# Optimization experiments

Hardware: AMD Instinct MI355X
Metric: run time of the kernel (lower is better)

Reference implementation:

```python
import jax, jax.numpy as jnp
import numpy as np

B, S, D = 32, 256, 768
H = 12
HD = D // H           # 64
MLP = 4 * D           # 3072
EPS = 1e-5


def layernorm(x, g, b):
    mu = jnp.mean(x, axis=-1, keepdims=True)
    var = jnp.mean((x - mu) ** 2, axis=-1, keepdims=True)
    return (x - mu) * jax.lax.rsqrt(var + EPS) * g + b


def setup_inputs() -> dict:
    key = jax.random.key(0)
    ks = jax.random.split(key, 16)
    s_head = 1.0 / np.sqrt(HD)
    s_d = 1.0 / np.sqrt(D)
    s_mlp = 1.0 / np.sqrt(MLP)
    return {
        "x": jax.random.normal(ks[0], (B, S, D), dtype=jnp.float32),
        "g1": jnp.ones((D,), jnp.float32),
        "beta1": jnp.zeros((D,), jnp.float32),
        # per-head linear weights, torch Linear layout [out, in] stacked over heads
        "Wq": jax.random.uniform(ks[1], (H, HD, HD), jnp.float32, -s_head, s_head),
        "bq": jax.random.uniform(ks[2], (H, HD), jnp.float32, -s_head, s_head),
        "Wk": jax.random.uniform(ks[3], (H, HD, HD), jnp.float32, -s_head, s_head),
        "bk": jax.random.uniform(ks[4], (H, HD), jnp.float32, -s_head, s_head),
        "Wv": jax.random.uniform(ks[5], (H, HD, HD), jnp.float32, -s_head, s_head),
        "bv": jax.random.uniform(ks[6], (H, HD), jnp.float32, -s_head, s_head),
        "g2": jnp.ones((D,), jnp.float32),
        "beta2": jnp.zeros((D,), jnp.float32),
        "W1": jax.random.uniform(ks[7], (MLP, D), jnp.float32, -s_d, s_d),
        "bm1": jax.random.uniform(ks[8], (MLP,), jnp.float32, -s_d, s_d),
        "W2": jax.random.uniform(ks[9], (D, MLP), jnp.float32, -s_mlp, s_mlp),
        "bm2": jax.random.uniform(ks[10], (D,), jnp.float32, -s_mlp, s_mlp),
    }


def reference(x, g1, beta1, Wq, bq, Wk, bk, Wv, bv, g2, beta2, W1, bm1, W2, bm2):
    # --- MHA on norm1(x), fused over batch and heads ---
    h = layernorm(x, g1, beta1)                      # [B,S,D]
    hh = h.reshape(B, S, H, HD)                      # head split matches slicing in Mymha
    # q_e = sum_d hh_d * W[e,d]  (torch Linear: y = x @ W.T + b)
    q = jnp.einsum('bshd,hed->bshe', hh, Wq) + bq
    k = jnp.einsum('bshd,hed->bshe', hh, Wk) + bk
    v = jnp.einsum('bshd,hed->bshe', hh, Wv) + bv
    scores = jnp.einsum('bshe,bthe->bhst', q, k) / np.sqrt(HD)
    attn = jax.nn.softmax(scores, axis=-1)           # [B,H,S,S]
    ctx = jnp.einsum('bhst,bthe->bshe', attn, v).reshape(B, S, D)
    out = ctx + x
    # --- MLP on norm2(out) ---
    h2 = layernorm(out, g2, beta2)
    m = jax.nn.gelu(h2 @ W1.T + bm1, approximate=False)  # torch nn.GELU is exact erf
    out = m @ W2.T + bm2 + out
    return out
```

## Files before the change

### kernel.cpp

```cpp
#include <hip/hip_runtime.h>
#include <hip/hip_bf16.h>
#include <math.h>


static constexpr int Bn = 32, Sn = 256, Dn = 768, Hn = 12, HDn = 64, MLPn = 3072;
static constexpr int NT = Bn * Sn;

typedef unsigned short ushort_t;
typedef unsigned int u32;
typedef __attribute__((ext_vector_type(8))) short short8;
typedef __attribute__((ext_vector_type(4))) float f32x4;

__device__ __forceinline__ float bf2f(ushort_t u) { return __uint_as_float(((u32)u) << 16); }
__device__ __forceinline__ ushort_t f2bf(float f) {
  u32 u = __float_as_uint(f);
  u += 0x7fffu + ((u >> 16) & 1u);
  return (ushort_t)(u >> 16);
}

__device__ __forceinline__ void async_cp16(const ushort_t* g, ushort_t* l) {
  __builtin_amdgcn_global_load_lds(
      (const __attribute__((address_space(1))) u32*)g,
      (__attribute__((address_space(3))) u32*)l, 16, 0, 0);
}

__global__ __launch_bounds__(256) void k_prep(
    const float* __restrict__ Wq, const float* __restrict__ Wk,
    const float* __restrict__ Wv, const float* __restrict__ bq,
    const float* __restrict__ bk, const float* __restrict__ bv,
    const float* __restrict__ W1, const float* __restrict__ W2,
    const float* __restrict__ x, const float* __restrict__ g1,
    const float* __restrict__ be1,
    ushort_t* __restrict__ Wc, float* __restrict__ bc,
    ushort_t* __restrict__ W1b, ushort_t* __restrict__ W2b,
    ushort_t* __restrict__ hb)
{
  __shared__ float red[8];
  const int bx = blockIdx.x;
  const int tid = threadIdx.x;
  if (bx < 576) {
    int i = bx * 256 + tid;
    int h = i / 12288, rem = i - h * 12288;
    int mat = rem / 4096, w = rem - mat * 4096;
    const float* src = (mat == 0) ? Wq : ((mat == 1) ? Wk : Wv);
    Wc[i] = f2bf(src[h * 4096 + w]);
    if (i < Hn * 192) {
      int h2 = i / 192, r2 = i - h2 * 192;
      int m2 = r2 / 64, e2 = r2 - m2 * 64;
      const float* bs = (m2 == 0) ? bq : ((m2 == 1) ? bk : bv);
      bc[i] = bs[h2 * 64 + e2];
    }
  } else if (bx < 5184) {
    int j = bx - 576;
    const float* src = (j < 2304) ? W1 : W2;
    ushort_t* dst = (j < 2304) ? W1b : W2b;
    int i = (j % 2304) * 256 + tid;
    float4 v = ((const float4*)src)[i];
    ushort4 o;
    o.x = f2bf(v.x); o.y = f2bf(v.y); o.z = f2bf(v.z); o.w = f2bf(v.w);
    ((ushort4*)dst)[i] = o;
  } else {
    const int t = bx - 5184;
    float xv[3];
#pragma unroll
    for (int i = 0; i < 3; i++) xv[i] = x[(size_t)t * Dn + tid + i * 256];
    float s = xv[0] + xv[1] + xv[2];
#pragma unroll
    for (int off = 32; off > 0; off >>= 1) s += __shfl_down(s, off, 64);
    if ((tid & 63) == 0) red[tid >> 6] = s;
    __syncthreads();
    float mean = (red[0] + red[1] + red[2] + red[3]) * (1.0f / 768.0f);
    float d0 = xv[0] - mean, d1 = xv[1] - mean, d2 = xv[2] - mean;
    float s2 = d0 * d0 + d1 * d1 + d2 * d2;
#pragma unroll
    for (int off = 32; off > 0; off >>= 1) s2 += __shfl_down(s2, off, 64);
    if ((tid & 63) == 0) red[4 + (tid >> 6)] = s2;
    __syncthreads();
    float rstd = rsqrtf((red[4] + red[5] + red[6] + red[7]) * (1.0f / 768.0f) + 1e-5f);
#pragma unroll
    for (int i = 0; i < 3; i++) {
      int d = tid + i * 256;
      hb[(size_t)t * Dn + d] = f2bf((xv[i] - mean) * rstd * g1[d] + be1[d]);
    }
  }
}

__global__ __launch_bounds__(256) void k_qkv(
    const ushort_t* __restrict__ hb,
    const ushort_t* __restrict__ Wc,
    const float* __restrict__ bc,
    ushort_t* __restrict__ qo, ushort_t* __restrict__ ko, ushort_t* __restrict__ vt)
{
  __shared__ __align__(16) ushort_t As[128 * 72];
  __shared__ __align__(16) ushort_t Ws[192 * 72];
  const int blk = blockIdx.x;
  const int half = blk & 1;
  const int bh = blk >> 1;
  const int b_ = bh / Hn, h_ = bh - b_ * Hn;
  const int tid = threadIdx.x;
  const int t0 = b_ * Sn + half * 128;

  {
    int row = tid >> 1, seg = (tid & 1) * 32;
    const uint4* g = (const uint4*)(hb + (size_t)(t0 + row) * Dn + h_ * 64 + seg);
    uint4* s = (uint4*)(As + row * 72 + seg);
    s[0] = g[0]; s[1] = g[1]; s[2] = g[2]; s[3] = g[3];
  }
  {
    int rr = tid >> 2, seg = (tid & 3) * 16;
    const ushort_t* gw = Wc + h_ * 12288;
#pragma unroll
    for (int p = 0; p < 3; p++) {
      int R = p * 64 + rr;
      const uint4* g = (const uint4*)(gw + R * 64 + seg);
      uint4* s = (uint4*)(Ws + R * 72 + seg);
      s[0] = g[0]; s[1] = g[1];
    }
  }
  __syncthreads();

  const int wave = tid >> 6, lane = tid & 63;
  const int wm = (wave >> 1) * 64, wn = (wave & 1) * 96;
  const int lrow = lane & 15, quad = lane >> 4;

  f32x4 acc[4][6];
#pragma unroll
  for (int mi = 0; mi < 4; mi++)
#pragma unroll
    for (int ni = 0; ni < 6; ni++) acc[mi][ni] = (f32x4){0.f, 0.f, 0.f, 0.f};

#pragma unroll
  for (int kk = 0; kk < 2; kk++) {
    short8 af[4], wf[6];
#pragma unroll
    for (int mi = 0; mi < 4; mi++)
      af[mi] = *(const short8*)(As + (wm + mi * 16 + lrow) * 72 + kk * 32 + quad * 8);
#pragma unroll
    for (int ni = 0; ni < 6; ni++)
      wf[ni] = *(const short8*)(Ws + (wn + ni * 16 + lrow) * 72 + kk * 32 + quad * 8);
#pragma unroll
    for (int mi = 0; mi < 4; mi++)
#pragma unroll
      for (int ni = 0; ni < 6; ni++)
        acc[mi][ni] = __builtin_amdgcn_mfma_f32_16x16x32_bf16(af[mi], wf[ni], acc[mi][ni], 0, 0, 0);
  }

#pragma unroll
  for (int ni = 0; ni < 6; ni++) {
    int c = wn + ni * 16 + lrow;
    int mat = c >> 6, e = c & 63;
    float bb = bc[h_ * 192 + c];
    if (mat < 2) {
      ushort_t* dst = (mat == 0) ? qo : ko;
      size_t base = (((size_t)bh) * Sn + half * 128 + wm) * HDn + e;
#pragma unroll
      for (int mi = 0; mi < 4; mi++) {
#pragma unroll
        for (int r = 0; r < 4; r++) {
          int lr = mi * 16 + quad * 4 + r;
          dst[base + (size_t)lr * HDn] = f2bf(acc[mi][ni][r] + bb);
        }
      }
    } else {
      size_t rowb = ((size_t)bh * 64 + e) * Sn + half * 128 + wm + quad * 4;
#pragma unroll
      for (int mi = 0; mi < 4; mi++) {
        ushort4 pk;
        pk.x = f2bf(acc[mi][ni][0] + bb);
        pk.y = f2bf(acc[mi][ni][1] + bb);
        pk.z = f2bf(acc[mi][ni][2] + bb);
        pk.w = f2bf(acc[mi][ni][3] + bb);
        *(ushort4*)(vt + rowb + mi * 16) = pk;
      }
    }
  }
}

__global__ __launch_bounds__(256) void k_attn(
    const ushort_t* __restrict__ q,
    const ushort_t* __restrict__ kg_,
    const ushort_t* __restrict__ vt,
    const float* __restrict__ x,
    float* __restrict__ out1)
{
  __shared__ __align__(16) ushort_t Ks[64 * 72];
  __shared__ __align__(16) ushort_t Vts[64 * 264];
  __shared__ __align__(16) ushort_t Pw[4][16 * 72];
  const int blk = blockIdx.x;
  const int qtr = blk & 3, bh = blk >> 2;
  const int b_ = bh / Hn, h_ = bh - b_ * Hn;
  const int tid = threadIdx.x, wave = tid >> 6, lane = tid & 63;
  const int lr16 = lane & 15, quad = lane >> 4;
  const int s0 = qtr * 64 + wave * 16;

  {
    int r = tid >> 2, cseg = (tid & 3) * 64;
    const uint4* g = (const uint4*)(vt + ((size_t)bh * 64 + r) * Sn + cseg);
    uint4* s = (uint4*)(Vts + r * 264 + cseg);
#pragma unroll
    for (int i = 0; i < 8; i++) s[i] = g[i];
  }

  short8 qf[2];
  {
    const ushort_t* qg = q + ((size_t)bh * Sn + s0 + lr16) * HDn + quad * 8;
    qf[0] = *(const short8*)(qg);
    qf[1] = *(const short8*)(qg + 32);
  }

  f32x4 of[4];
#pragma unroll
  for (int et = 0; et < 4; et++) of[et] = (f32x4){0.f, 0.f, 0.f, 0.f};
  float mrow[4] = {-3.0e38f, -3.0e38f, -3.0e38f, -3.0e38f};
  float lsum[4] = {0.f, 0.f, 0.f, 0.f};

  const ushort_t* kgb = kg_ + (size_t)bh * Sn * HDn;

  for (int c = 0; c < 4; c++) {
    if (c) __syncthreads();
    {
      int row = tid >> 2, seg = (tid & 3) * 16;
      const uint4* g = (const uint4*)(kgb + (size_t)(c * 64 + row) * HDn + seg);
      uint4* s = (uint4*)(Ks + row * 72 + seg);
      s[0] = g[0]; s[1] = g[1];
    }
    __syncthreads();

    f32x4 sc[4];
#pragma unroll
    for (int ni = 0; ni < 4; ni++) sc[ni] = (f32x4){0.f, 0.f, 0.f, 0.f};
#pragma unroll
    for (int kk = 0; kk < 2; kk++) {
#pragma unroll
      for (int ni = 0; ni < 4; ni++) {
        short8 kf = *(const short8*)(Ks + (ni * 16 + lr16) * 72 + kk * 32 + quad * 8);
        sc[ni] = __builtin_amdgcn_mfma_f32_16x16x32_bf16(qf[kk], kf, sc[ni], 0, 0, 0);
      }
    }

    float alpha[4];
#pragma unroll
    for (int r = 0; r < 4; r++) {
      float m_ = fmaxf(fmaxf(sc[0][r], sc[1][r]), fmaxf(sc[2][r], sc[3][r]));
#pragma unroll
      for (int msk = 8; msk >= 1; msk >>= 1) m_ = fmaxf(m_, __shfl_xor(m_, msk, 64));
      float mn = fmaxf(mrow[r], m_);
      alpha[r] = __expf((mrow[r] - mn) * 0.125f);
      mrow[r] = mn;
    }
#pragma unroll
    for (int ni = 0; ni < 4; ni++) {
#pragma unroll
      for (int r = 0; r < 4; r++) {
        float p = __expf((sc[ni][r] - mrow[r]) * 0.125f);
        sc[ni][r] = p;
        Pw[wave][(quad * 4 + r) * 72 + ni * 16 + lr16] = f2bf(p);
      }
    }
#pragma unroll
    for (int r = 0; r < 4; r++) {
      float s_ = (sc[0][r] + sc[1][r]) + (sc[2][r] + sc[3][r]);
#pragma unroll
      for (int msk = 8; msk >= 1; msk >>= 1) s_ += __shfl_xor(s_, msk, 64);
      lsum[r] = lsum[r] * alpha[r] + s_;
    }
#pragma unroll
    for (int et = 0; et < 4; et++)
#pragma unroll
      for (int r = 0; r < 4; r++) of[et][r] *= alpha[r];

    short8 pf0 = *(const short8*)(&Pw[wave][lr16 * 72 + quad * 8]);
    short8 pf1 = *(const short8*)(&Pw[wave][lr16 * 72 + 32 + quad * 8]);
#pragma unroll
    for (int et = 0; et < 4; et++) {
      short8 vf0 = *(const short8*)(Vts + (et * 16 + lr16) * 264 + c * 64 + quad * 8);
      short8 vf1 = *(const short8*)(Vts + (et * 16 + lr16) * 264 + c * 64 + 32 + quad * 8);
      of[et] = __builtin_amdgcn_mfma_f32_16x16x32_bf16(pf0, vf0, of[et], 0, 0, 0);
      of[et] = __builtin_amdgcn_mfma_f32_16x16x32_bf16(pf1, vf1, of[et], 0, 0, 0);
    }
  }

  const size_t obase = ((size_t)b_ * Sn + s0) * Dn + h_ * 64;
#pragma unroll
  for (int r = 0; r < 4; r++) {
    float rl = 1.0f / lsum[r];
    int row = quad * 4 + r;
#pragma unroll
    for (int et = 0; et < 4; et++) {
      size_t idx = obase + (size_t)row * Dn + et * 16 + lr16;
      out1[idx] = of[et][r] * rl + x[idx];
    }
  }
}

__global__ __launch_bounds__(256) void k_ln2(
    const float* __restrict__ in, const float* __restrict__ g2,
    const float* __restrict__ be2, ushort_t* __restrict__ h2)
{
  const int t = blockIdx.x, tid = threadIdx.x;
  __shared__ float red[8];
  float xv[3];
#pragma unroll
  for (int i = 0; i < 3; i++) xv[i] = in[(size_t)t * Dn + tid + i * 256];
  float s = xv[0] + xv[1] + xv[2];
#pragma unroll
  for (int off = 32; off > 0; off >>= 1) s += __shfl_down(s, off, 64);
  if ((tid & 63) == 0) red[tid >> 6] = s;
  __syncthreads();
  float mean = (red[0] + red[1] + red[2] + red[3]) * (1.0f / 768.0f);
  float d0 = xv[0] - mean, d1 = xv[1] - mean, d2 = xv[2] - mean;
  float s2 = d0 * d0 + d1 * d1 + d2 * d2;
#pragma unroll
  for (int off = 32; off > 0; off >>= 1) s2 += __shfl_down(s2, off, 64);
  if ((tid & 63) == 0) red[4 + (tid >> 6)] = s2;
  __syncthreads();
  float rstd = rsqrtf((red[4] + red[5] + red[6] + red[7]) * (1.0f / 768.0f) + 1e-5f);
#pragma unroll
  for (int i = 0; i < 3; i++) {
    int d = tid + i * 256;
    h2[(size_t)t * Dn + d] = f2bf((xv[i] - mean) * rstd * g2[d] + be2[d]);
  }
}

__global__ __launch_bounds__(512) void k_gemm1(
    const ushort_t* __restrict__ A,
    const ushort_t* __restrict__ Bw,
    const float* __restrict__ bias,
    ushort_t* __restrict__ CoutB)
{
  constexpr int KDIM = Dn, N = MLPn;
  __shared__ __align__(16) ushort_t smem[24576];
  ushort_t* Asb[2] = { smem, smem + 12288 };
  ushort_t* Bsb[2] = { smem + 8192, smem + 20480 };
  ushort_t* Cs = smem;
  const int b = blockIdx.x;
  const int xcd = b & 7, slot = b >> 3;
  const int cc = slot % 24, rloc = slot / 24;
  const int m0 = (xcd * 4 + rloc) * 256, n0 = cc * 128;
  const int tid = threadIdx.x;
  const int wave = tid >> 6, lane = tid & 63;
  const int wm = (wave >> 1) << 6, wn = (wave & 1) << 6;
  const int lrow = lane & 15, quad = lane >> 4;
  const int lrow4 = lane >> 2, lcol8 = (lane & 3) * 8;

  f32x4 acc[4][4];
#pragma unroll
  for (int mi = 0; mi < 4; mi++)
#pragma unroll
    for (int ni = 0; ni < 4; ni++) acc[mi][ni] = (f32x4){0.f, 0.f, 0.f, 0.f};

  for (int k0 = 0; k0 < KDIM; k0 += 64) {
#pragma unroll
    for (int t = 0; t < 2; t++) {
      async_cp16(A + (size_t)(m0 + wave * 16 + lrow4) * KDIM + k0 + t * 32 + lcol8,
                 Asb[t] + (wave * 16) * 32);
      async_cp16(A + (size_t)(m0 + 128 + wave * 16 + lrow4) * KDIM + k0 + t * 32 + lcol8,
                 Asb[t] + (128 + wave * 16) * 32);
      async_cp16(Bw + (size_t)(n0 + wave * 16 + lrow4) * KDIM + k0 + t * 32 + lcol8,
                 Bsb[t] + (wave * 16) * 32);
    }
    __syncthreads();
#pragma unroll
    for (int t = 0; t < 2; t++) {
      short8 af[4], bfv[4];
#pragma unroll
      for (int mi = 0; mi < 4; mi++)
        af[mi] = *(const short8*)(Asb[t] + (wm + mi * 16 + lrow) * 32 + quad * 8);
#pragma unroll
      for (int ni = 0; ni < 4; ni++)
        bfv[ni] = *(const short8*)(Bsb[t] + (wn + ni * 16 + lrow) * 32 + quad * 8);
#pragma unroll
      for (int mi = 0; mi < 4; mi++)
#pragma unroll
        for (int ni = 0; ni < 4; ni++)
          acc[mi][ni] = __builtin_amdgcn_mfma_f32_16x16x32_bf16(af[mi], bfv[ni], acc[mi][ni], 0, 0, 0);
    }
    __syncthreads();
  }

#pragma unroll
  for (int p = 0; p < 2; p++) {
    if ((wm >> 7) == p) {
#pragma unroll
      for (int ni = 0; ni < 4; ni++) {
        int col = wn + ni * 16 + lrow;
        float bc = bias[n0 + col];
#pragma unroll
        for (int mi = 0; mi < 4; mi++) {
#pragma unroll
          for (int r = 0; r < 4; r++) {
            float vv = acc[mi][ni][r] + bc;
            float u = vv * (0.7978845608f + 0.0356774081f * vv * vv);
            float o = vv / (1.0f + __expf(-2.0f * u));
            Cs[((wm & 127) + mi * 16 + quad * 4 + r) * 136 + col] = f2bf(o);
          }
        }
      }
    }
    __syncthreads();
    int row = tid >> 2, part = tid & 3;
    const uint4* s = (const uint4*)(Cs + row * 136 + part * 32);
    uint4* d = (uint4*)(CoutB + (size_t)(m0 + p * 128 + row) * N + n0 + part * 32);
#pragma unroll
    for (int i = 0; i < 4; i++) d[i] = s[i];
    if (p == 0) __syncthreads();
  }
}

__global__ __launch_bounds__(256) void k_gemm2(
    const ushort_t* __restrict__ A,
    const ushort_t* __restrict__ Bw,
    const float* __restrict__ bias,
    const float* __restrict__ res,
    float* __restrict__ out)
{
  constexpr int KDIM = MLPn, N = Dn;
  __shared__ __align__(16) ushort_t As[2][64 * 32];
  __shared__ __align__(16) ushort_t Bs[2][128 * 32];
  const int b = blockIdx.x;
  const int xcd = b & 7, slot = b >> 3;
  const int cc = slot % 6, rloc = slot / 6;
  const int m0 = (xcd * 16 + rloc) * 64, n0 = cc * 128;
  const int tid = threadIdx.x;
  const int wave = tid >> 6, lane = tid & 63;
  const int wm = (wave >> 1) << 5, wn = (wave & 1) << 6;
  const int lrow = lane & 15, quad = lane >> 4;
  const int lrow4 = lane >> 2, lcol8 = (lane & 3) * 8;

  f32x4 acc[2][4];
#pragma unroll
  for (int mi = 0; mi < 2; mi++)
#pragma unroll
    for (int ni = 0; ni < 4; ni++) acc[mi][ni] = (f32x4){0.f, 0.f, 0.f, 0.f};

  for (int k0 = 0; k0 < KDIM; k0 += 64) {
#pragma unroll
    for (int t = 0; t < 2; t++) {
      int rr = wave * 16;
      async_cp16(A + (size_t)(m0 + rr + lrow4) * KDIM + k0 + t * 32 + lcol8, As[t] + rr * 32);
#pragma unroll
      for (int a = 0; a < 2; a++) {
        int rb = rr + a * 64;
        async_cp16(Bw + (size_t)(n0 + rb + lrow4) * KDIM + k0 + t * 32 + lcol8, Bs[t] + rb * 32);
      }
    }
    __syncthreads();
#pragma unroll
    for (int t = 0; t < 2; t++) {
      short8 af[2], bfv[4];
#pragma unroll
      for (int mi = 0; mi < 2; mi++)
        af[mi] = *(const short8*)(As[t] + (wm + mi * 16 + lrow) * 32 + quad * 8);
#pragma unroll
      for (int ni = 0; ni < 4; ni++)
        bfv[ni] = *(const short8*)(Bs[t] + (wn + ni * 16 + lrow) * 32 + quad * 8);
#pragma unroll
      for (int mi = 0; mi < 2; mi++)
#pragma unroll
        for (int ni = 0; ni < 4; ni++)
          acc[mi][ni] = __builtin_amdgcn_mfma_f32_16x16x32_bf16(af[mi], bfv[ni], acc[mi][ni], 0, 0, 0);
    }
    __syncthreads();
  }

#pragma unroll
  for (int ni = 0; ni < 4; ni++) {
    int col = n0 + wn + ni * 16 + lrow;
    float bc = bias[col];
#pragma unroll
    for (int mi = 0; mi < 2; mi++) {
#pragma unroll
      for (int r = 0; r < 4; r++) {
        int row = m0 + wm + mi * 16 + quad * 4 + r;
        size_t idx = (size_t)row * N + col;
        out[idx] = acc[mi][ni][r] + bc + res[idx];
      }
    }
  }
}

extern "C" void kernel_launch(void* const* d_in, const int* in_sizes, int n_in,
                              void* d_out, int out_size, void* d_ws, size_t ws_size,
                              hipStream_t stream) {
  (void)in_sizes; (void)n_in; (void)out_size; (void)ws_size;
  const float* x   = (const float*)d_in[0];
  const float* g1  = (const float*)d_in[1];
  const float* be1 = (const float*)d_in[2];
  const float* Wq  = (const float*)d_in[3];
  const float* bq  = (const float*)d_in[4];
  const float* Wk  = (const float*)d_in[5];
  const float* bk  = (const float*)d_in[6];
  const float* Wv  = (const float*)d_in[7];
  const float* bv  = (const float*)d_in[8];
  const float* g2  = (const float*)d_in[9];
  const float* be2 = (const float*)d_in[10];
  const float* W1  = (const float*)d_in[11];
  const float* bm1 = (const float*)d_in[12];
  const float* W2  = (const float*)d_in[13];
  const float* bm2 = (const float*)d_in[14];
  float* outp = (float*)d_out;

  char* ws = (char*)d_ws;
  float*    out1 = (float*)ws;
  ushort_t* hb   = (ushort_t*)ws;
  ushort_t* qb   = (ushort_t*)(ws + 25165824);
  ushort_t* kb   = (ushort_t*)(ws + 37748736);
  ushort_t* vtb  = (ushort_t*)(ws + 50331648);
  ushort_t* h2   = qb;
  ushort_t* mb   = (ushort_t*)(ws + 37748736);
  ushort_t* Wc   = (ushort_t*)(ws + 88080384);
  ushort_t* W1b  = (ushort_t*)(ws + 88375296);
  ushort_t* W2b  = (ushort_t*)(ws + 93093888);
  float*    bcb  = (float*)(ws + 97812480);

  k_prep<<<dim3(5184 + NT), dim3(256), 0, stream>>>(Wq, Wk, Wv, bq, bk, bv, W1, W2,
                                                    x, g1, be1, Wc, bcb, W1b, W2b, hb);
  k_qkv<<<dim3(Bn * Hn * 2), dim3(256), 0, stream>>>(hb, Wc, bcb, qb, kb, vtb);
  k_attn<<<dim3(Bn * Hn * 4), dim3(256), 0, stream>>>(qb, kb, vtb, x, out1);
  k_ln2<<<dim3(NT), dim3(256), 0, stream>>>(out1, g2, be2, h2);
  k_gemm1<<<dim3(768), dim3(512), 0, stream>>>(h2, W1b, bm1, mb);
  k_gemm2<<<dim3(768), dim3(256), 0, stream>>>(mb, W2b, bm2, out1, outp);
}
```

Before: 297.7 us.

## Double-buffer MLP GEMM tiles with async prefetch and XOR-swizzled LDS layout

Both MLP GEMM kernels now prefetch the next K-slice into a second LDS buffer while MFMAs run on the current one, so global-to-LDS loads overlap compute instead of being exposed behind a barrier each iteration. LDS tile columns are XOR-swizzled on the async copy and on the fragment reads to cut bank conflicts. gemm2 also widens its LDS rows to 64 elements (two MFMA k-steps per stage) and moves to a larger shared buffer. The risks are correctness of the swizzle and prefetch indexing, and possible occupancy loss from the larger LDS footprint in gemm2.

```diff
diff --git a/kernel.cpp b/kernel.cpp
--- a/kernel.cpp
+++ b/kernel.cpp
@@ -330,8 +330,10 @@
 {
   constexpr int KDIM = Dn, N = MLPn;
   __shared__ __align__(16) ushort_t smem[24576];
-  ushort_t* Asb[2] = { smem, smem + 12288 };
-  ushort_t* Bsb[2] = { smem + 8192, smem + 20480 };
+  ushort_t* As0 = smem;
+  ushort_t* Bs0 = smem + 8192;
+  ushort_t* As1 = smem + 12288;
+  ushort_t* Bs1 = smem + 20480;
   ushort_t* Cs = smem;
   const int b = blockIdx.x;
   const int xcd = b & 7, slot = b >> 3;
@@ -341,7 +343,9 @@
   const int wave = tid >> 6, lane = tid & 63;
   const int wm = (wave >> 1) << 6, wn = (wave & 1) << 6;
   const int lrow = lane & 15, quad = lane >> 4;
-  const int lrow4 = lane >> 2, lcol8 = (lane & 3) * 8;
+  const int lrow4 = lane >> 2;
+  const int lcol8s = (((lane & 3) ^ ((lane >> 3) & 3))) * 8;
+  const int qsw = ((quad ^ ((lrow >> 1) & 3))) * 8;
 
   f32x4 acc[4][4];
 #pragma unroll
@@ -349,32 +353,37 @@
 #pragma unroll
     for (int ni = 0; ni < 4; ni++) acc[mi][ni] = (f32x4){0.f, 0.f, 0.f, 0.f};
 
+  auto stage = [&](int k0, ushort_t* Ad, ushort_t* Bd) {
+    async_cp16(A + (size_t)(m0 + wave * 16 + lrow4) * KDIM + k0 + lcol8s,
+               Ad + (wave * 16) * 32);
+    async_cp16(A + (size_t)(m0 + 128 + wave * 16 + lrow4) * KDIM + k0 + lcol8s,
+               Ad + (128 + wave * 16) * 32);
+    async_cp16(Bw + (size_t)(n0 + wave * 16 + lrow4) * KDIM + k0 + lcol8s,
+               Bd + (wave * 16) * 32);
+  };
+  auto compute = [&](const ushort_t* As_, const ushort_t* Bs_) {
+    short8 af[4], bfv[4];
+#pragma unroll
+    for (int mi = 0; mi < 4; mi++)
+      af[mi] = *(const short8*)(As_ + (wm + mi * 16 + lrow) * 32 + qsw);
+#pragma unroll
+    for (int ni = 0; ni < 4; ni++)
+      bfv[ni] = *(const short8*)(Bs_ + (wn + ni * 16 + lrow) * 32 + qsw);
+#pragma unroll
+    for (int mi = 0; mi < 4; mi++)
+#pragma unroll
+      for (int ni = 0; ni < 4; ni++)
+        acc[mi][ni] = __builtin_amdgcn_mfma_f32_16x16x32_bf16(af[mi], bfv[ni], acc[mi][ni], 0, 0, 0);
+  };
+
+  stage(0, As0, Bs0);
+  __syncthreads();
   for (int k0 = 0; k0 < KDIM; k0 += 64) {
-#pragma unroll
-    for (int t = 0; t < 2; t++) {
-      async_cp16(A + (size_t)(m0 + wave * 16 + lrow4) * KDIM + k0 + t * 32 + lcol8,
-                 Asb[t] + (wave * 16) * 32);
-      async_cp16(A + (size_t)(m0 + 128 + wave * 16 + lrow4) * KDIM + k0 + t * 32 + lcol8,
-                 Asb[t] + (128 + wave * 16) * 32);
-      async_cp16(Bw + (size_t)(n0 + wave * 16 + lrow4) * KDIM + k0 + t * 32 + lcol8,
-                 Bsb[t] + (wave * 16) * 32);
-    }
-    __syncthreads();
-#pragma unroll
-    for (int t = 0; t < 2; t++) {
-      short8 af[4], bfv[4];
-#pragma unroll
-      for (int mi = 0; mi < 4; mi++)
-        af[mi] = *(const short8*)(Asb[t] + (wm + mi * 16 + lrow) * 32 + quad * 8);
-#pragma unroll
-      for (int ni = 0; ni < 4; ni++)
-        bfv[ni] = *(const short8*)(Bsb[t] + (wn + ni * 16 + lrow) * 32 + quad * 8);
-#pragma unroll
-      for (int mi = 0; mi < 4; mi++)
-#pragma unroll
-        for (int ni = 0; ni < 4; ni++)
-          acc[mi][ni] = __builtin_amdgcn_mfma_f32_16x16x32_bf16(af[mi], bfv[ni], acc[mi][ni], 0, 0, 0);
-    }
+    stage(k0 + 32, As1, Bs1);
+    compute(As0, Bs0);
+    __syncthreads();
+    if (k0 + 64 < KDIM) stage(k0 + 64, As0, Bs0);
+    compute(As1, Bs1);
     __syncthreads();
   }
 
@@ -415,8 +424,11 @@
     float* __restrict__ out)
 {
   constexpr int KDIM = MLPn, N = Dn;
-  __shared__ __align__(16) ushort_t As[2][64 * 32];
-  __shared__ __align__(16) ushort_t Bs[2][128 * 32];
+  __shared__ __align__(16) ushort_t smem[24576];
+  ushort_t* As0 = smem;
+  ushort_t* Bs0 = smem + 4096;
+  ushort_t* As1 = smem + 12288;
+  ushort_t* Bs1 = smem + 16384;
   const int b = blockIdx.x;
   const int xcd = b & 7, slot = b >> 3;
   const int cc = slot % 6, rloc = slot / 6;
@@ -425,7 +437,10 @@
   const int wave = tid >> 6, lane = tid & 63;
   const int wm = (wave >> 1) << 5, wn = (wave & 1) << 6;
   const int lrow = lane & 15, quad = lane >> 4;
-  const int lrow4 = lane >> 2, lcol8 = (lane & 3) * 8;
+  const int r8 = lane >> 3;
+  const int c8s = (((lane & 7) ^ ((lane >> 3) & 7))) * 8;
+  const int qsw2[2] = { ((0 * 4 + quad) ^ (lrow & 7)) * 8,
+                        ((1 * 4 + quad) ^ (lrow & 7)) * 8 };
 
   f32x4 acc[2][4];
 #pragma unroll
@@ -433,33 +448,42 @@
 #pragma unroll
     for (int ni = 0; ni < 4; ni++) acc[mi][ni] = (f32x4){0.f, 0.f, 0.f, 0.f};
 
-  for (int k0 = 0; k0 < KDIM; k0 += 64) {
-#pragma unroll
-    for (int t = 0; t < 2; t++) {
-      int rr = wave * 16;
-      async_cp16(A + (size_t)(m0 + rr + lrow4) * KDIM + k0 + t * 32 + lcol8, As[t] + rr * 32);
-#pragma unroll
-      for (int a = 0; a < 2; a++) {
-        int rb = rr + a * 64;
-        async_cp16(Bw + (size_t)(n0 + rb + lrow4) * KDIM + k0 + t * 32 + lcol8, Bs[t] + rb * 32);
-      }
-    }
-    __syncthreads();
-#pragma unroll
-    for (int t = 0; t < 2; t++) {
+  auto stage = [&](int k0, ushort_t* Ad, ushort_t* Bd) {
+    async_cp16(A + (size_t)(m0 + wave * 8 + r8) * KDIM + k0 + c8s,
+               Ad + (wave * 8) * 64);
+    async_cp16(A + (size_t)(m0 + 32 + wave * 8 + r8) * KDIM + k0 + c8s,
+               Ad + (32 + wave * 8) * 64);
+#pragma unroll
+    for (int g = 0; g < 4; g++)
+      async_cp16(Bw + (size_t)(n0 + g * 32 + wave * 8 + r8) * KDIM + k0 + c8s,
+                 Bd + (g * 32 + wave * 8) * 64);
+  };
+  auto compute = [&](const ushort_t* As_, const ushort_t* Bs_) {
+#pragma unroll
+    for (int kk = 0; kk < 2; kk++) {
       short8 af[2], bfv[4];
 #pragma unroll
       for (int mi = 0; mi < 2; mi++)
-        af[mi] = *(const short8*)(As[t] + (wm + mi * 16 + lrow) * 32 + quad * 8);
+        af[mi] = *(const short8*)(As_ + (wm + mi * 16 + lrow) * 64 + qsw2[kk]);
 #pragma unroll
       for (int ni = 0; ni < 4; ni++)
-        bfv[ni] = *(const short8*)(Bs[t] + (wn + ni * 16 + lrow) * 32 + quad * 8);
+        bfv[ni] = *(const short8*)(Bs_ + (wn + ni * 16 + lrow) * 64 + qsw2[kk]);
 #pragma unroll
       for (int mi = 0; mi < 2; mi++)
 #pragma unroll
         for (int ni = 0; ni < 4; ni++)
           acc[mi][ni] = __builtin_amdgcn_mfma_f32_16x16x32_bf16(af[mi], bfv[ni], acc[mi][ni], 0, 0, 0);
     }
+  };
+
+  stage(0, As0, Bs0);
+  __syncthreads();
+  for (int k0 = 0; k0 < KDIM; k0 += 128) {
+    stage(k0 + 64, As1, Bs1);
+    compute(As0, Bs0);
+    __syncthreads();
+    if (k0 + 128 < KDIM) stage(k0 + 128, As0, Bs0);
+    compute(As1, Bs1);
     __syncthreads();
   }
 
```

Result: faster. 286.2 us (-3.9%).
